# Optimization experiments

Measured on AMD Instinct MI355X. Metric: run time of the kernel, lower is better.

The kernel has to match this reference:

```python
import jax, jax.numpy as jnp
import numpy as np

H = 16  # heads
DH = 64  # dim_head
SCALE = DH ** -0.5


def rotate_half(x):
    x1, x2 = jnp.split(x, 2, axis=-1)
    return jnp.concatenate([-x2, x1], axis=-1)


def apply_rope(pos, t):
    # pos: [n, d] broadcast over [b, h, n, d]
    return t * jnp.cos(pos) + rotate_half(t) * jnp.sin(pos)


def setup_inputs() -> dict:
    key = jax.random.key(0)
    ks = jax.random.split(key, 6)
    B, N, D = 4, 2048, 1024
    inner = H * DH
    x = jax.random.normal(ks[0], (B, N, D), dtype=jnp.float32)
    rotary_emb = jax.random.normal(ks[1], (N, DH), dtype=jnp.float32)
    Wq = jax.random.normal(ks[2], (D, inner), dtype=jnp.float32) / np.sqrt(D)
    Wkv = jax.random.normal(ks[3], (D, 2 * inner), dtype=jnp.float32) / np.sqrt(D)
    Wout = jax.random.normal(ks[4], (inner, D), dtype=jnp.float32) / np.sqrt(inner)
    bout = jnp.zeros((D,), dtype=jnp.float32)
    return {"x": x, "rotary_emb": rotary_emb, "Wq": Wq, "Wkv": Wkv, "Wout": Wout, "bout": bout}


def reference(x, rotary_emb, Wq, Wkv, Wout, bout):
    B, N, D = x.shape
    # QKV projections (self-attention: context = x)
    q = x @ Wq                       # [b, n, h*d]
    kv = x @ Wkv                     # [b, n, 2*h*d]
    k, v = jnp.split(kv, 2, axis=-1)

    def to_heads(t):
        return t.reshape(B, N, H, DH).transpose(0, 2, 1, 3)  # [b, h, n, d]

    q, k, v = to_heads(q), to_heads(k), to_heads(v)
    q = apply_rope(rotary_emb, q)
    k = apply_rope(rotary_emb, k)

    # scaled dot-product attention
    scores = jnp.einsum('bhid,bhjd->bhij', q, k) * SCALE
    attn = jax.nn.softmax(scores, axis=-1)
    out = jnp.einsum('bhij,bhjd->bhid', attn, v)  # [b, h, n, d]
    out = out.transpose(0, 2, 1, 3).reshape(B, N, H * DH)
    return out @ Wout + bout
```

## Files before the change

kernel.cpp:

```cpp
#include <hip/hip_runtime.h>

#define BB 4
#define NN 2048
#define DD 1024
#define HH 16
#define DHH 64
#define MM (BB*NN)
#define QS 3072

typedef unsigned short u16;
typedef __attribute__((ext_vector_type(8))) short short8;
typedef __attribute__((ext_vector_type(4))) float floatx4;

#if __has_builtin(__builtin_amdgcn_exp2f)
#define EXP2F __builtin_amdgcn_exp2f
#else
#define EXP2F exp2f
#endif

__device__ __forceinline__ u16 f2bf(float f) {
  union { float f; unsigned u; } v; v.f = f;
  unsigned u = v.u;
  return (u16)((u + 0x7fffu + ((u >> 16) & 1u)) >> 16);
}
__device__ __forceinline__ float bf2f(u16 h) {
  union { unsigned u; float f; } v; v.u = ((unsigned)h) << 16;
  return v.f;
}
__device__ __forceinline__ unsigned fbits(float f) {
  union { float f; unsigned u; } v; v.f = f; return v.u;
}
__device__ __forceinline__ unsigned pkbf(float lo, float hi) {
  unsigned a = fbits(lo) + 0x8000u;
  unsigned b = fbits(hi) + 0x8000u;
#if __has_builtin(__builtin_amdgcn_perm)
  return __builtin_amdgcn_perm(b, a, 0x07060302u);
#else
  return (a >> 16) | (b & 0xffff0000u);
#endif
}
__device__ __forceinline__ void gll16(const u16* g, u16* l) {
  __builtin_amdgcn_global_load_lds((const __attribute__((address_space(1))) unsigned int*)g,
                                   (__attribute__((address_space(3))) unsigned int*)l, 16, 0, 0);
}

__global__ __launch_bounds__(256) void cvt_kernel(const float* __restrict__ in,
                                                  u16* __restrict__ out, int n) {
  int i = (blockIdx.x * 256 + threadIdx.x) * 4;
  if (i >= n) return;
  float4 v = *(const float4*)(in + i);
  u16 o[4] = {f2bf(v.x), f2bf(v.y), f2bf(v.z), f2bf(v.w)};
  *(uint2*)(out + i) = *(uint2*)o;
}

__global__ __launch_bounds__(256) void tcvt_kernel(const float* __restrict__ in,
                                                   u16* __restrict__ out, int R, int C) {
  __shared__ float t[64][65];
  int r0 = blockIdx.y * 64, c0 = blockIdx.x * 64;
  int tid = threadIdx.x;
#pragma unroll
  for (int i = 0; i < 16; ++i) {
    int lin = i * 256 + tid;
    int rr = lin >> 6, cc = lin & 63;
    t[rr][cc] = in[(size_t)(r0 + rr) * C + c0 + cc];
  }
  __syncthreads();
#pragma unroll
  for (int i = 0; i < 16; ++i) {
    int lin = i * 256 + tid;
    int rr = lin >> 6, cc = lin & 63;
    out[(size_t)(c0 + rr) * R + r0 + cc] = f2bf(t[cc][rr]);
  }
}

__global__ __launch_bounds__(256) void rope_tab_kernel(const float* __restrict__ rot,
                                                       float2* __restrict__ tab) {
  int i = blockIdx.x * 256 + threadIdx.x;
  float p = rot[i];
  float s, c;
  __sincosf(p, &s, &c);
  tab[i] = make_float2(c, s);
}

__global__ __launch_bounds__(256) void gemm_qkv(const u16* __restrict__ A,
                                                const u16* __restrict__ Bt,
                                                u16* __restrict__ qd,
                                                u16* __restrict__ kd,
                                                u16* __restrict__ vt,
                                                const float2* __restrict__ tab) {
  const int K = DD;
  __shared__ __align__(16) u16 As[128 * 32];
  __shared__ __align__(16) u16 Bs[128 * 32];
  int tid = threadIdx.x;
  int wave = tid >> 6, lane = tid & 63;
  int q4 = lane >> 4, l16 = lane & 15;
  int m0 = blockIdx.y * 128, n0 = blockIdx.x * 128;
  int wm = (wave >> 1) * 64, wn = (wave & 1) * 64;

  int srow = wave * 16 + (lane >> 2);
  int schunk = (lane & 3) * 8;
  u16* ldsA0 = As + wave * 512;  u16* ldsA1 = As + (4 + wave) * 512;
  u16* ldsB0 = Bs + wave * 512;  u16* ldsB1 = Bs + (4 + wave) * 512;
  const u16* Ag = A + (size_t)m0 * K;
  const u16* Bg = Bt + (size_t)n0 * K;

  floatx4 acc[4][4];
#pragma unroll
  for (int mi = 0; mi < 4; ++mi)
#pragma unroll
    for (int ni = 0; ni < 4; ++ni) acc[mi][ni] = (floatx4){0.f, 0.f, 0.f, 0.f};

  for (int k0 = 0; k0 < K; k0 += 32) {
    __syncthreads();
    gll16(Ag + (size_t)srow * K + k0 + schunk, ldsA0);
    gll16(Ag + (size_t)(srow + 64) * K + k0 + schunk, ldsA1);
    gll16(Bg + (size_t)srow * K + k0 + schunk, ldsB0);
    gll16(Bg + (size_t)(srow + 64) * K + k0 + schunk, ldsB1);
    __syncthreads();
    short8 af[4], bfr[4];
#pragma unroll
    for (int i = 0; i < 4; ++i) {
      af[i]  = *(const short8*)(As + (wm + i * 16 + l16) * 32 + q4 * 8);
      bfr[i] = *(const short8*)(Bs + (wn + i * 16 + l16) * 32 + q4 * 8);
    }
#pragma unroll
    for (int mi = 0; mi < 4; ++mi)
#pragma unroll
      for (int ni = 0; ni < 4; ++ni)
        acc[mi][ni] = __builtin_amdgcn_mfma_f32_16x16x32_bf16(af[mi], bfr[ni], acc[mi][ni], 0, 0, 0);
  }

  int colbase = n0 + wn;
  int slot = colbase >> 10;
  int h = (colbase >> 6) & 15;
#pragma unroll
  for (int mi = 0; mi < 4; ++mi) {
    int mbase = m0 + wm + mi * 16 + q4 * 4;
    float vals[4][4];
    if (slot < 2) {
#pragma unroll
      for (int r = 0; r < 4; ++r) {
        int n = (mbase + r) & (NN - 1);
#pragma unroll
        for (int ni = 0; ni < 2; ++ni) {
          int d0 = ni * 16 + l16;
          float2 cs0 = tab[n * 64 + d0];
          float2 cs1 = tab[n * 64 + d0 + 32];
          float v0 = acc[mi][ni][r], v1 = acc[mi][ni + 2][r];
          vals[ni][r]     = v0 * cs0.x - v1 * cs0.y;
          vals[ni + 2][r] = v1 * cs1.x + v0 * cs1.y;
        }
      }
      u16* dst = slot ? kd : qd;
#pragma unroll
      for (int ni = 0; ni < 4; ++ni)
#pragma unroll
        for (int r = 0; r < 4; ++r) {
          int m = mbase + r;
          dst[((size_t)((m >> 11) * HH + h) * NN + (m & (NN - 1))) * 64 + ni * 16 + l16] =
              f2bf(vals[ni][r]);
        }
    } else {
#pragma unroll
      for (int ni = 0; ni < 4; ++ni) {
        int d = ni * 16 + l16;
#pragma unroll
        for (int r = 0; r < 4; ++r) {
          int m = mbase + r;
          int nn = m & (NN - 1);
          vt[(size_t)((m >> 11) * HH + h) * (NN * 64) + (nn >> 6) * 4096 + d * 64 + (nn & 63)] =
              f2bf(acc[mi][ni][r]);
        }
      }
    }
  }
}

__global__ __launch_bounds__(256) void gemm_out(const u16* __restrict__ A,
                                                const u16* __restrict__ Bt,
                                                float* __restrict__ Cout,
                                                const float* __restrict__ bias,
                                                int M, int N, int K) {
  __shared__ __align__(16) u16 As[128 * 32];
  __shared__ __align__(16) u16 Bs[128 * 32];
  int tid = threadIdx.x;
  int wave = tid >> 6, lane = tid & 63;
  int q4 = lane >> 4, l16 = lane & 15;
  int m0 = blockIdx.y * 128, n0 = blockIdx.x * 128;
  int wm = (wave >> 1) * 64, wn = (wave & 1) * 64;

  int srow = wave * 16 + (lane >> 2);
  int schunk = (lane & 3) * 8;
  u16* ldsA0 = As + wave * 512;  u16* ldsA1 = As + (4 + wave) * 512;
  u16* ldsB0 = Bs + wave * 512;  u16* ldsB1 = Bs + (4 + wave) * 512;
  const u16* Ag = A + (size_t)m0 * K;
  const u16* Bg = Bt + (size_t)n0 * K;

  floatx4 acc[4][4];
#pragma unroll
  for (int mi = 0; mi < 4; ++mi)
#pragma unroll
    for (int ni = 0; ni < 4; ++ni) acc[mi][ni] = (floatx4){0.f, 0.f, 0.f, 0.f};

  for (int k0 = 0; k0 < K; k0 += 32) {
    __syncthreads();
    gll16(Ag + (size_t)srow * K + k0 + schunk, ldsA0);
    gll16(Ag + (size_t)(srow + 64) * K + k0 + schunk, ldsA1);
    gll16(Bg + (size_t)srow * K + k0 + schunk, ldsB0);
    gll16(Bg + (size_t)(srow + 64) * K + k0 + schunk, ldsB1);
    __syncthreads();
    short8 af[4], bfr[4];
#pragma unroll
    for (int i = 0; i < 4; ++i) {
      af[i]  = *(const short8*)(As + (wm + i * 16 + l16) * 32 + q4 * 8);
      bfr[i] = *(const short8*)(Bs + (wn + i * 16 + l16) * 32 + q4 * 8);
    }
#pragma unroll
    for (int mi = 0; mi < 4; ++mi)
#pragma unroll
      for (int ni = 0; ni < 4; ++ni)
        acc[mi][ni] = __builtin_amdgcn_mfma_f32_16x16x32_bf16(af[mi], bfr[ni], acc[mi][ni], 0, 0, 0);
  }

#pragma unroll
  for (int ni = 0; ni < 4; ++ni) {
    int col = n0 + wn + ni * 16 + l16;
    float bval = bias[col];
#pragma unroll
    for (int mi = 0; mi < 4; ++mi) {
#pragma unroll
      for (int r = 0; r < 4; ++r) {
        int row = m0 + wm + mi * 16 + q4 * 4 + r;
        Cout[(size_t)row * N + col] = acc[mi][ni][r] + bval;
      }
    }
  }
}

__global__ __launch_bounds__(512, 4) void attn_kernel(const u16* __restrict__ qd,
                                                      const u16* __restrict__ kd,
                                                      const u16* __restrict__ vt,
                                                      u16* __restrict__ ao) {
  __shared__ __align__(16) u16 lds[16384];

  int tid = threadIdx.x, wave = tid >> 6, lane = tid & 63;
  int q4 = lane >> 4, l16 = lane & 15;
  int qt = blockIdx.x, bh = blockIdx.y, b = bh >> 4, h = bh & 15;
  const u16* qbh = qd + (size_t)bh * NN * 64;
  const u16* kbh = kd + (size_t)bh * NN * 64;
  const u16* vbh = vt + (size_t)bh * NN * 64;

  int srow = wave * 8 + (lane >> 3);
  int g = ((lane & 7) ^ ((lane >> 3) & 7)) * 8;
  int prow = ((srow >> 2) & 3) * 8 + ((srow >> 4) & 1) * 4 + (srow & 3) + ((srow >> 5) & 1) * 32;

#pragma unroll
  for (int it = 0; it < 4; ++it)
    gll16(qbh + (size_t)(qt * 256 + it * 64 + srow) * 64 + g, lds + (it * 64 + wave * 8) * 64);
  __builtin_amdgcn_s_waitcnt(0x0F70);
  __builtin_amdgcn_s_barrier();

  short8 aq[2][2];
#pragma unroll
  for (int mi = 0; mi < 2; ++mi)
#pragma unroll
    for (int ks = 0; ks < 2; ++ks) {
      int row = wave * 32 + mi * 16 + l16;
      aq[mi][ks] = *(const short8*)(lds + row * 64 + (((ks * 4 + q4) ^ (row & 7)) * 8));
    }
  __builtin_amdgcn_s_waitcnt(0xC07F);
  __builtin_amdgcn_s_barrier();

  gll16(kbh + (size_t)prow * 64 + g, lds + wave * 512);
  gll16(vbh + (size_t)srow * 64 + g, lds + 8192 + wave * 512);

  float lsum[2] = {0.f, 0.f};
  floatx4 o[2][4];
#pragma unroll
  for (int mi = 0; mi < 2; ++mi)
#pragma unroll
    for (int di = 0; di < 4; ++di) o[mi][di] = (floatx4){0.f, 0.f, 0.f, 0.f};

  for (int j0 = 0, itn = 0; j0 < NN; j0 += 64, ++itn) {
    int coff = (itn & 1) * 4096;
    if (j0 + 64 < NN) {
      int noff = 4096 - coff;
      gll16(kbh + (size_t)(j0 + 64 + prow) * 64 + g, lds + noff + wave * 512);
      gll16(vbh + (size_t)((j0 >> 6) + 1) * 4096 + srow * 64 + g, lds + 8192 + noff + wave * 512);
      __builtin_amdgcn_s_waitcnt(0x0F72);
    } else {
      __builtin_amdgcn_s_waitcnt(0x0F70);
    }
    __builtin_amdgcn_s_barrier();

    const u16* Kc = lds + coff;
    const u16* Vc = lds + 8192 + coff;

    floatx4 s[4][2];
#pragma unroll
    for (int kg = 0; kg < 4; ++kg)
#pragma unroll
      for (int mi = 0; mi < 2; ++mi) s[kg][mi] = (floatx4){0.f, 0.f, 0.f, 0.f};
#pragma unroll
    for (int ks = 0; ks < 2; ++ks) {
      short8 kf[4];
#pragma unroll
      for (int kg = 0; kg < 4; ++kg) {
        int row = kg * 16 + l16;
        kf[kg] = *(const short8*)(Kc + row * 64 + (((ks * 4 + q4) ^ (row & 7)) * 8));
      }
#pragma unroll
      for (int kg = 0; kg < 4; ++kg)
#pragma unroll
        for (int mi = 0; mi < 2; ++mi)
          s[kg][mi] = __builtin_amdgcn_mfma_f32_16x16x32_bf16(kf[kg], aq[mi][ks], s[kg][mi], 0, 0, 0);
    }

    unsigned pk[4][2][2];
#pragma unroll
    for (int kg = 0; kg < 4; ++kg)
#pragma unroll
      for (int mi = 0; mi < 2; ++mi) {
        float e0 = EXP2F(fmaf(s[kg][mi][0], 0.18033688f, -28.8539008f));
        float e1 = EXP2F(fmaf(s[kg][mi][1], 0.18033688f, -28.8539008f));
        float e2 = EXP2F(fmaf(s[kg][mi][2], 0.18033688f, -28.8539008f));
        float e3 = EXP2F(fmaf(s[kg][mi][3], 0.18033688f, -28.8539008f));
        lsum[mi] += (e0 + e1) + (e2 + e3);
        pk[kg][mi][0] = pkbf(e0, e1);
        pk[kg][mi][1] = pkbf(e2, e3);
      }

#pragma unroll
    for (int ks = 0; ks < 2; ++ks) {
      short8 vf[4];
#pragma unroll
      for (int di = 0; di < 4; ++di) {
        int row = di * 16 + l16;
        vf[di] = *(const short8*)(Vc + row * 64 + (((ks * 4 + q4) ^ (row & 7)) * 8));
      }
#pragma unroll
      for (int mi = 0; mi < 2; ++mi) {
        union { unsigned u[4]; short8 s8; } bw;
        bw.u[0] = pk[2 * ks][mi][0];
        bw.u[1] = pk[2 * ks][mi][1];
        bw.u[2] = pk[2 * ks + 1][mi][0];
        bw.u[3] = pk[2 * ks + 1][mi][1];
#pragma unroll
        for (int di = 0; di < 4; ++di)
          o[mi][di] = __builtin_amdgcn_mfma_f32_16x16x32_bf16(vf[di], bw.s8, o[mi][di], 0, 0, 0);
      }
    }
    __builtin_amdgcn_s_barrier();
  }

  float rinv[2];
#pragma unroll
  for (int mi = 0; mi < 2; ++mi) {
    float v = lsum[mi];
    v += __shfl_xor(v, 16, 64);
    v += __shfl_xor(v, 32, 64);
    rinv[mi] = 1.0f / v;
  }

#pragma unroll
  for (int mi = 0; mi < 2; ++mi) {
    int qrow = qt * 256 + wave * 32 + mi * 16 + l16;
    size_t base = (size_t)(b * NN + qrow) * DD + h * DHH + q4 * 4;
#pragma unroll
    for (int di = 0; di < 4; ++di)
#pragma unroll
      for (int r = 0; r < 4; ++r)
        ao[base + di * 16 + r] = f2bf(o[mi][di][r] * rinv[mi]);
  }
}

extern "C" void kernel_launch(void* const* d_in, const int* in_sizes, int n_in,
                              void* d_out, int out_size, void* d_ws, size_t ws_size,
                              hipStream_t stream) {
  const float* x    = (const float*)d_in[0];
  const float* rot  = (const float*)d_in[1];
  const float* Wq   = (const float*)d_in[2];
  const float* Wkv  = (const float*)d_in[3];
  const float* Wout = (const float*)d_in[4];
  const float* bout = (const float*)d_in[5];
  float* out = (float*)d_out;

  char* ws = (char*)d_ws;
  size_t off = 0;
  auto alloc = [&](size_t bytes) {
    void* p = ws + off;
    off = (off + bytes + 255) & ~(size_t)255;
    return p;
  };
  u16*    xb    = (u16*)alloc((size_t)MM * DD * 2);
  u16*    WT    = (u16*)alloc((size_t)QS * DD * 2);
  u16*    WoutT = (u16*)alloc((size_t)DD * DD * 2);
  float2* tab   = (float2*)alloc((size_t)NN * DHH * 8);
  u16*    qdb   = (u16*)alloc((size_t)MM * DD * 2);
  u16*    kdb   = (u16*)alloc((size_t)MM * DD * 2);
  u16*    vtt   = (u16*)alloc((size_t)MM * DD * 2);
  u16*    ao    = (u16*)alloc((size_t)MM * DD * 2);

  cvt_kernel<<<(MM * DD / 4) / 256, 256, 0, stream>>>(x, xb, MM * DD);
  tcvt_kernel<<<dim3(DD / 64, DD / 64), 256, 0, stream>>>(Wq, WT, DD, DD);
  tcvt_kernel<<<dim3(2 * DD / 64, DD / 64), 256, 0, stream>>>(Wkv, WT + (size_t)DD * DD, DD, 2 * DD);
  tcvt_kernel<<<dim3(DD / 64, DD / 64), 256, 0, stream>>>(Wout, WoutT, DD, DD);
  rope_tab_kernel<<<(NN * DHH) / 256, 256, 0, stream>>>(rot, tab);

  gemm_qkv<<<dim3(QS / 128, MM / 128), 256, 0, stream>>>(xb, WT, qdb, kdb, vtt, tab);

  attn_kernel<<<dim3(NN / 256, BB * HH), 512, 0, stream>>>(qdb, kdb, vtt, ao);

  gemm_out<<<dim3(DD / 128, MM / 128), 256, 0, stream>>>(ao, WoutT, out, bout, MM, DD, DD);
}
```

Measured before the change: 300.0 us.

## Double-buffer GEMM LDS loads with swizzled layout and merge weight transposes

Both GEMM kernels now use two LDS stages: the global-to-LDS loads for the next K tile are issued before computing on the current one, with an explicit waitcnt and barrier replacing the two __syncthreads per iteration. The LDS tile uses an XOR-swizzled layout that pairs rows, which should cut bank conflicts on the MFMA fragment reads. The three weight transpose-convert launches are folded into one kernel to save launch overhead. Risks are the hand-coded waitcnt encodings and the doubled LDS footprint per block, which may lower occupancy.

```diff
diff --git a/kernel.cpp b/kernel.cpp
--- a/kernel.cpp
+++ b/kernel.cpp
@@ -43,6 +43,11 @@
   __builtin_amdgcn_global_load_lds((const __attribute__((address_space(1))) unsigned int*)g,
                                    (__attribute__((address_space(3))) unsigned int*)l, 16, 0, 0);
 }
+__device__ __forceinline__ int toff(int row, int kc) {
+  int pr = row >> 1;
+  int c = (((row & 1) << 2) + kc) ^ (pr & 7);
+  return pr * 64 + c * 8;
+}
 
 __global__ __launch_bounds__(256) void cvt_kernel(const float* __restrict__ in,
                                                   u16* __restrict__ out, int n) {
@@ -53,23 +58,34 @@
   *(uint2*)(out + i) = *(uint2*)o;
 }
 
-__global__ __launch_bounds__(256) void tcvt_kernel(const float* __restrict__ in,
-                                                   u16* __restrict__ out, int R, int C) {
+__global__ __launch_bounds__(256) void tcvt3_kernel(const float* __restrict__ Wq,
+                                                    const float* __restrict__ Wkv,
+                                                    const float* __restrict__ Wout,
+                                                    u16* __restrict__ WT,
+                                                    u16* __restrict__ WoutT) {
   __shared__ float t[64][65];
-  int r0 = blockIdx.y * 64, c0 = blockIdx.x * 64;
+  int bx = blockIdx.x;
+  const float* src;
+  u16* dst;
+  int C, c0;
+  if (bx < 16)      { src = Wq;   dst = WT;                       C = 1024; c0 = bx * 64; }
+  else if (bx < 48) { src = Wkv;  dst = WT + (size_t)DD * DD;     C = 2048; c0 = (bx - 16) * 64; }
+  else              { src = Wout; dst = WoutT;                    C = 1024; c0 = (bx - 48) * 64; }
+  const int R = 1024;
+  int r0 = blockIdx.y * 64;
   int tid = threadIdx.x;
 #pragma unroll
   for (int i = 0; i < 16; ++i) {
     int lin = i * 256 + tid;
     int rr = lin >> 6, cc = lin & 63;
-    t[rr][cc] = in[(size_t)(r0 + rr) * C + c0 + cc];
+    t[rr][cc] = src[(size_t)(r0 + rr) * C + c0 + cc];
   }
   __syncthreads();
 #pragma unroll
   for (int i = 0; i < 16; ++i) {
     int lin = i * 256 + tid;
     int rr = lin >> 6, cc = lin & 63;
-    out[(size_t)(c0 + rr) * R + r0 + cc] = f2bf(t[cc][rr]);
+    dst[(size_t)(c0 + rr) * R + r0 + cc] = f2bf(t[cc][rr]);
   }
 }
 
@@ -89,20 +105,28 @@
                                                 u16* __restrict__ vt,
                                                 const float2* __restrict__ tab) {
   const int K = DD;
-  __shared__ __align__(16) u16 As[128 * 32];
-  __shared__ __align__(16) u16 Bs[128 * 32];
+  __shared__ __align__(16) u16 lds[16384];
   int tid = threadIdx.x;
   int wave = tid >> 6, lane = tid & 63;
   int q4 = lane >> 4, l16 = lane & 15;
   int m0 = blockIdx.y * 128, n0 = blockIdx.x * 128;
   int wm = (wave >> 1) * 64, wn = (wave & 1) * 64;
 
-  int srow = wave * 16 + (lane >> 2);
-  int schunk = (lane & 3) * 8;
-  u16* ldsA0 = As + wave * 512;  u16* ldsA1 = As + (4 + wave) * 512;
-  u16* ldsB0 = Bs + wave * 512;  u16* ldsB1 = Bs + (4 + wave) * 512;
   const u16* Ag = A + (size_t)m0 * K;
   const u16* Bg = Bt + (size_t)n0 * K;
+  int o1 = tid, o2 = tid + 256;
+  int pr1 = o1 >> 3, c1 = (o1 & 7) ^ (pr1 & 7);
+  int row1 = pr1 * 2 + (c1 >> 2), kc1 = (c1 & 3) * 8;
+  int pr2 = o2 >> 3, c2 = (o2 & 7) ^ (pr2 & 7);
+  int row2 = pr2 * 2 + (c2 >> 2), kc2 = (c2 & 3) * 8;
+  int d1 = wave * 512, d2 = 2048 + wave * 512;
+
+  int foA[4], foB[4];
+#pragma unroll
+  for (int i = 0; i < 4; ++i) {
+    foA[i] = toff(wm + i * 16 + l16, q4);
+    foB[i] = toff(wn + i * 16 + l16, q4);
+  }
 
   floatx4 acc[4][4];
 #pragma unroll
@@ -110,24 +134,39 @@
 #pragma unroll
     for (int ni = 0; ni < 4; ++ni) acc[mi][ni] = (floatx4){0.f, 0.f, 0.f, 0.f};
 
-  for (int k0 = 0; k0 < K; k0 += 32) {
-    __syncthreads();
-    gll16(Ag + (size_t)srow * K + k0 + schunk, ldsA0);
-    gll16(Ag + (size_t)(srow + 64) * K + k0 + schunk, ldsA1);
-    gll16(Bg + (size_t)srow * K + k0 + schunk, ldsB0);
-    gll16(Bg + (size_t)(srow + 64) * K + k0 + schunk, ldsB1);
-    __syncthreads();
+  gll16(Ag + (size_t)row1 * K + kc1, lds + d1);
+  gll16(Ag + (size_t)row2 * K + kc2, lds + d2);
+  gll16(Bg + (size_t)row1 * K + kc1, lds + 8192 + d1);
+  gll16(Bg + (size_t)row2 * K + kc2, lds + 8192 + d2);
+
+  for (int k0 = 0, it = 0; k0 < K; k0 += 32, ++it) {
+    int boff = (it & 1) * 4096;
+    if (k0 + 32 < K) {
+      int nboff = 4096 - boff;
+      int kn = k0 + 32;
+      gll16(Ag + (size_t)row1 * K + kn + kc1, lds + nboff + d1);
+      gll16(Ag + (size_t)row2 * K + kn + kc2, lds + nboff + d2);
+      gll16(Bg + (size_t)row1 * K + kn + kc1, lds + 8192 + nboff + d1);
+      gll16(Bg + (size_t)row2 * K + kn + kc2, lds + 8192 + nboff + d2);
+      __builtin_amdgcn_s_waitcnt(0x0F74);
+    } else {
+      __builtin_amdgcn_s_waitcnt(0x0F70);
+    }
+    __builtin_amdgcn_s_barrier();
+    const u16* Ac = lds + boff;
+    const u16* Bc = lds + 8192 + boff;
     short8 af[4], bfr[4];
 #pragma unroll
     for (int i = 0; i < 4; ++i) {
-      af[i]  = *(const short8*)(As + (wm + i * 16 + l16) * 32 + q4 * 8);
-      bfr[i] = *(const short8*)(Bs + (wn + i * 16 + l16) * 32 + q4 * 8);
+      af[i]  = *(const short8*)(Ac + foA[i]);
+      bfr[i] = *(const short8*)(Bc + foB[i]);
     }
 #pragma unroll
     for (int mi = 0; mi < 4; ++mi)
 #pragma unroll
       for (int ni = 0; ni < 4; ++ni)
         acc[mi][ni] = __builtin_amdgcn_mfma_f32_16x16x32_bf16(af[mi], bfr[ni], acc[mi][ni], 0, 0, 0);
+    __builtin_amdgcn_s_barrier();
   }
 
   int colbase = n0 + wn;
@@ -181,20 +220,28 @@
                                                 float* __restrict__ Cout,
                                                 const float* __restrict__ bias,
                                                 int M, int N, int K) {
-  __shared__ __align__(16) u16 As[128 * 32];
-  __shared__ __align__(16) u16 Bs[128 * 32];
+  __shared__ __align__(16) u16 lds[16384];
   int tid = threadIdx.x;
   int wave = tid >> 6, lane = tid & 63;
   int q4 = lane >> 4, l16 = lane & 15;
   int m0 = blockIdx.y * 128, n0 = blockIdx.x * 128;
   int wm = (wave >> 1) * 64, wn = (wave & 1) * 64;
 
-  int srow = wave * 16 + (lane >> 2);
-  int schunk = (lane & 3) * 8;
-  u16* ldsA0 = As + wave * 512;  u16* ldsA1 = As + (4 + wave) * 512;
-  u16* ldsB0 = Bs + wave * 512;  u16* ldsB1 = Bs + (4 + wave) * 512;
   const u16* Ag = A + (size_t)m0 * K;
   const u16* Bg = Bt + (size_t)n0 * K;
+  int o1 = tid, o2 = tid + 256;
+  int pr1 = o1 >> 3, c1 = (o1 & 7) ^ (pr1 & 7);
+  int row1 = pr1 * 2 + (c1 >> 2), kc1 = (c1 & 3) * 8;
+  int pr2 = o2 >> 3, c2 = (o2 & 7) ^ (pr2 & 7);
+  int row2 = pr2 * 2 + (c2 >> 2), kc2 = (c2 & 3) * 8;
+  int d1 = wave * 512, d2 = 2048 + wave * 512;
+
+  int foA[4], foB[4];
+#pragma unroll
+  for (int i = 0; i < 4; ++i) {
+    foA[i] = toff(wm + i * 16 + l16, q4);
+    foB[i] = toff(wn + i * 16 + l16, q4);
+  }
 
   floatx4 acc[4][4];
 #pragma unroll
@@ -202,24 +249,39 @@
 #pragma unroll
     for (int ni = 0; ni < 4; ++ni) acc[mi][ni] = (floatx4){0.f, 0.f, 0.f, 0.f};
 
-  for (int k0 = 0; k0 < K; k0 += 32) {
-    __syncthreads();
-    gll16(Ag + (size_t)srow * K + k0 + schunk, ldsA0);
-    gll16(Ag + (size_t)(srow + 64) * K + k0 + schunk, ldsA1);
-    gll16(Bg + (size_t)srow * K + k0 + schunk, ldsB0);
-    gll16(Bg + (size_t)(srow + 64) * K + k0 + schunk, ldsB1);
-    __syncthreads();
+  gll16(Ag + (size_t)row1 * K + kc1, lds + d1);
+  gll16(Ag + (size_t)row2 * K + kc2, lds + d2);
+  gll16(Bg + (size_t)row1 * K + kc1, lds + 8192 + d1);
+  gll16(Bg + (size_t)row2 * K + kc2, lds + 8192 + d2);
+
+  for (int k0 = 0, it = 0; k0 < K; k0 += 32, ++it) {
+    int boff = (it & 1) * 4096;
+    if (k0 + 32 < K) {
+      int nboff = 4096 - boff;
+      int kn = k0 + 32;
+      gll16(Ag + (size_t)row1 * K + kn + kc1, lds + nboff + d1);
+      gll16(Ag + (size_t)row2 * K + kn + kc2, lds + nboff + d2);
+      gll16(Bg + (size_t)row1 * K + kn + kc1, lds + 8192 + nboff + d1);
+      gll16(Bg + (size_t)row2 * K + kn + kc2, lds + 8192 + nboff + d2);
+      __builtin_amdgcn_s_waitcnt(0x0F74);
+    } else {
+      __builtin_amdgcn_s_waitcnt(0x0F70);
+    }
+    __builtin_amdgcn_s_barrier();
+    const u16* Ac = lds + boff;
+    const u16* Bc = lds + 8192 + boff;
     short8 af[4], bfr[4];
 #pragma unroll
     for (int i = 0; i < 4; ++i) {
-      af[i]  = *(const short8*)(As + (wm + i * 16 + l16) * 32 + q4 * 8);
-      bfr[i] = *(const short8*)(Bs + (wn + i * 16 + l16) * 32 + q4 * 8);
+      af[i]  = *(const short8*)(Ac + foA[i]);
+      bfr[i] = *(const short8*)(Bc + foB[i]);
     }
 #pragma unroll
     for (int mi = 0; mi < 4; ++mi)
 #pragma unroll
       for (int ni = 0; ni < 4; ++ni)
         acc[mi][ni] = __builtin_amdgcn_mfma_f32_16x16x32_bf16(af[mi], bfr[ni], acc[mi][ni], 0, 0, 0);
+    __builtin_amdgcn_s_barrier();
   }
 
 #pragma unroll
@@ -402,9 +464,7 @@
   u16*    ao    = (u16*)alloc((size_t)MM * DD * 2);
 
   cvt_kernel<<<(MM * DD / 4) / 256, 256, 0, stream>>>(x, xb, MM * DD);
-  tcvt_kernel<<<dim3(DD / 64, DD / 64), 256, 0, stream>>>(Wq, WT, DD, DD);
-  tcvt_kernel<<<dim3(2 * DD / 64, DD / 64), 256, 0, stream>>>(Wkv, WT + (size_t)DD * DD, DD, 2 * DD);
-  tcvt_kernel<<<dim3(DD / 64, DD / 64), 256, 0, stream>>>(Wout, WoutT, DD, DD);
+  tcvt3_kernel<<<dim3(64, 16), 256, 0, stream>>>(Wq, Wkv, Wout, WT, WoutT);
   rope_tab_kernel<<<(NN * DHH) / 256, 256, 0, stream>>>(rot, tab);
 
   gemm_qkv<<<dim3(QS / 128, MM / 128), 256, 0, stream>>>(xb, WT, qdb, kdb, vtt, tab);
```

Measured after the change: 274.1 us. 8.6% less time.
